# Optimization experiments

Hardware: AMD Instinct MI355X
Metric: run time of the kernel (lower is better)

## Reference

```python
import jax, jax.numpy as jnp
import numpy as np

N_NODES = 50000
N_EDGES = 800000
D_IN = 512
D_OUT = 256


def setup_inputs() -> dict:
    key = jax.random.key(0)
    k1, k2, k3 = jax.random.split(key, 3)
    x = jax.random.normal(k1, (N_NODES, D_IN), dtype=jnp.float32)
    edge_index = jax.random.randint(k2, (2, N_EDGES), 0, N_NODES, dtype=jnp.int64)
    # Glorot-style init for the GCN weight, zero bias (PyG defaults)
    W = jax.random.normal(k3, (D_IN, D_OUT), dtype=jnp.float32) * (1.0 / np.sqrt(D_IN))
    b = jnp.zeros((D_OUT,), dtype=jnp.float32)
    return {"x": x, "edge_index": edge_index, "W": W, "b": b}


def reference(x, edge_index, W, b):
    N = x.shape[0]
    # 1) dense linear transform (the compute-heavy GEMM)
    xw = x @ W  # [N, d_out]

    # 2) add self-loops (PyG GCNConv default)
    loop = jnp.arange(N, dtype=edge_index.dtype)
    row = jnp.concatenate([edge_index[0], loop])  # sources
    col = jnp.concatenate([edge_index[1], loop])  # targets

    # 3) symmetric normalization deg^{-1/2} on targets (in-degree incl. self-loops)
    deg = jax.ops.segment_sum(jnp.ones_like(col, dtype=xw.dtype), col, num_segments=N)
    dinv = jnp.where(deg > 0, jax.lax.rsqrt(deg), 0.0)
    norm = dinv[row] * dinv[col]  # [E+N]

    # 4) gather source features, scale, scatter-add to targets
    msgs = xw[row] * norm[:, None]  # [E+N, d_out]
    agg = jax.ops.segment_sum(msgs, col, num_segments=N)  # [N, d_out]

    # 5) bias + ReLU (dropout is identity in eval mode)
    return jax.nn.relu(agg + b)
```

## Files before the change

### kernel.cpp

```cpp
#include <hip/hip_runtime.h>
#include <hip/hip_bf16.h>

#define N_NODES 50000
#define N_EDGES 800000
#define D_IN    512
#define D_OUT   256
#define NBLK_SCAN ((N_NODES + 1023) / 1024)

typedef short s8v  __attribute__((ext_vector_type(8)));
typedef float f32x4 __attribute__((ext_vector_type(4)));

__device__ __forceinline__ unsigned short bf16b(float f) {
    __hip_bfloat16 h = __float2bfloat16(f);
    return *reinterpret_cast<unsigned short*>(&h);
}

__device__ __forceinline__ int wave_incl_scan(int v, int lane) {
    #pragma unroll
    for (int d = 1; d < 64; d <<= 1) {
        int u = __shfl_up(v, d, 64);
        if (lane >= d) v += u;
    }
    return v;
}


__global__ void k_count(const int* __restrict__ col, int* __restrict__ cnt) {
    int i = blockIdx.x * 256 + threadIdx.x;
    if (i < N_EDGES) atomicAdd(&cnt[col[i]], 1);
}

__launch_bounds__(256)
__global__ void k_scan1(const int* __restrict__ cnt, int* __restrict__ bsum) {
    const int t = threadIdx.x, b = blockIdx.x;
    const int idx = b * 1024 + t * 4;
    int4 v = make_int4(0, 0, 0, 0);
    if (idx < N_NODES) v = *(const int4*)&cnt[idx];
    int s = v.x + v.y + v.z + v.w;
    #pragma unroll
    for (int d = 1; d < 64; d <<= 1) s += __shfl_xor(s, d, 64);
    __shared__ int ws[4];
    if ((t & 63) == 0) ws[t >> 6] = s;
    __syncthreads();
    if (t == 0) bsum[b] = ws[0] + ws[1] + ws[2] + ws[3];
}

__global__ void k_scan2(const int* __restrict__ bsum, int* __restrict__ boff) {
    const int t = threadIdx.x;
    int v = (t < NBLK_SCAN) ? bsum[t] : 0;
    int inc = wave_incl_scan(v, t);
    if (t < NBLK_SCAN) boff[t] = inc - v;
}

__launch_bounds__(256)
__global__ void k_scan3(const int* __restrict__ cnt, const int* __restrict__ boff,
                        int* __restrict__ row_ptr, float* __restrict__ dinv,
                        int* __restrict__ cursor) {
    const int t = threadIdx.x, b = blockIdx.x;
    const int lane = t & 63, wv = t >> 6;
    const int idx = b * 1024 + t * 4;
    int4 v = make_int4(0, 0, 0, 0);
    if (idx < N_NODES) v = *(const int4*)&cnt[idx];
    int s = v.x + v.y + v.z + v.w;
    int isc = wave_incl_scan(s, lane);
    __shared__ int wsum[4];
    if (lane == 63) wsum[wv] = isc;
    __syncthreads();
    int off = boff[b];
    #pragma unroll
    for (int i = 0; i < 4; ++i)
        if (i < wv) off += wsum[i];
    int p0 = off + isc - s;
    int p1 = p0 + v.x;
    int p2 = p1 + v.y;
    int p3 = p2 + v.z;
    if (idx < N_NODES) {
        row_ptr[idx + 0] = p0; cursor[idx + 0] = p0; dinv[idx + 0] = rsqrtf(1.f + (float)v.x);
        row_ptr[idx + 1] = p1; cursor[idx + 1] = p1; dinv[idx + 1] = rsqrtf(1.f + (float)v.y);
        row_ptr[idx + 2] = p2; cursor[idx + 2] = p2; dinv[idx + 2] = rsqrtf(1.f + (float)v.z);
        row_ptr[idx + 3] = p3; cursor[idx + 3] = p3; dinv[idx + 3] = rsqrtf(1.f + (float)v.w);
    }
    if (b == 0 && t == 0) row_ptr[N_NODES] = N_EDGES;
}

__global__ void k_fill(const int* __restrict__ row, const int* __restrict__ col,
                       int* __restrict__ cursor, int* __restrict__ csr_src) {
    int i = blockIdx.x * 256 + threadIdx.x;
    if (i < N_EDGES) {
        int pos = atomicAdd(&cursor[col[i]], 1);
        csr_src[pos] = row[i];
    }
}

__global__ void k_wt(const float* __restrict__ W, unsigned short* __restrict__ Wt) {
    int k = blockIdx.x;
    int n = threadIdx.x;
    Wt[(size_t)n * D_IN + k] = bf16b(W[(size_t)k * D_OUT + n]);
}

__launch_bounds__(256)
__global__ void k_gemm(const float* __restrict__ A,
                       const unsigned short* __restrict__ Wt,
                       const float* __restrict__ dinv,
                       unsigned short* __restrict__ yb)
{
    __shared__ __align__(16) unsigned short As[128 * 64];
    __shared__ __align__(16) unsigned short Bs[128 * 64];

    const int t  = threadIdx.x;
    const int nt = blockIdx.x & 1;
    const int mt = blockIdx.x >> 1;
    const int m0 = mt * 128;
    const int n0 = nt * 128;

    const int w  = t >> 6;
    const int l  = t & 63;
    const int wm = (w >> 1) * 64;
    const int wn = (w & 1) * 64;
    const int lr = l & 15;
    const int lk = l >> 4;

    const int sr   = t >> 3;
    const int skg  = t & 7;
    const int swz  = (sr & 7) << 4;
    const int aswz = (lr & 7) << 4;

    f32x4 acc[4][4] = {};

    for (int kk = 0; kk < D_IN; kk += 64) {
        #pragma unroll
        for (int i = 0; i < 4; ++i) {
            int m   = i * 32 + sr;
            int row = m0 + m;
            float4 v0 = make_float4(0.f,0.f,0.f,0.f), v1 = v0;
            if (row < N_NODES) {
                const float* src = &A[(size_t)row * D_IN + kk + skg * 8];
                v0 = *(const float4*)src;
                v1 = *(const float4*)(src + 4);
            }
            union { uint4 q; unsigned short h[8]; } pk;
            pk.h[0] = bf16b(v0.x); pk.h[1] = bf16b(v0.y);
            pk.h[2] = bf16b(v0.z); pk.h[3] = bf16b(v0.w);
            pk.h[4] = bf16b(v1.x); pk.h[5] = bf16b(v1.y);
            pk.h[6] = bf16b(v1.z); pk.h[7] = bf16b(v1.w);
            *(uint4*)((char*)As + ((m * 128 + skg * 16) ^ swz)) = pk.q;
        }
        #pragma unroll
        for (int i = 0; i < 4; ++i) {
            int n = i * 32 + sr;
            uint4 q = *(const uint4*)&Wt[(size_t)(n0 + n) * D_IN + kk + skg * 8];
            *(uint4*)((char*)Bs + ((n * 128 + skg * 16) ^ swz)) = q;
        }
        __syncthreads();

        #pragma unroll
        for (int ks = 0; ks < 2; ++ks) {
            const int kb = (ks * 64 + lk * 16) ^ aswz;
            s8v af[4], bfr[4];
            #pragma unroll
            for (int f = 0; f < 4; ++f)
                af[f]  = *(const s8v*)((const char*)As + ((wm + f * 16 + lr) * 128 + kb));
            #pragma unroll
            for (int f = 0; f < 4; ++f)
                bfr[f] = *(const s8v*)((const char*)Bs + ((wn + f * 16 + lr) * 128 + kb));
            #pragma unroll
            for (int fm = 0; fm < 4; ++fm)
                #pragma unroll
                for (int fn = 0; fn < 4; ++fn)
                    acc[fm][fn] = __builtin_amdgcn_mfma_f32_16x16x32_bf16(
                        af[fm], bfr[fn], acc[fm][fn], 0, 0, 0);
        }
        __syncthreads();
    }

    #pragma unroll
    for (int fm = 0; fm < 4; ++fm) {
        #pragma unroll
        for (int j = 0; j < 4; ++j) {
            int row = m0 + wm + fm * 16 + lk * 4 + j;
            if (row < N_NODES) {
                float s = dinv[row];
                #pragma unroll
                for (int fn = 0; fn < 4; ++fn) {
                    int col = n0 + wn + fn * 16 + lr;
                    yb[(size_t)row * D_OUT + col] = bf16b(acc[fm][fn][j] * s);
                }
            }
        }
    }
}

__device__ __forceinline__ void add8(float* acc, uint4 q) {
    unsigned x;
    x = q.x; acc[0] += __uint_as_float(x << 16); acc[1] += __uint_as_float(x & 0xffff0000u);
    x = q.y; acc[2] += __uint_as_float(x << 16); acc[3] += __uint_as_float(x & 0xffff0000u);
    x = q.z; acc[4] += __uint_as_float(x << 16); acc[5] += __uint_as_float(x & 0xffff0000u);
    x = q.w; acc[6] += __uint_as_float(x << 16); acc[7] += __uint_as_float(x & 0xffff0000u);
}

__launch_bounds__(256)
__global__ void k_gather(const int* __restrict__ row_ptr, const int* __restrict__ csr_src,
                         const unsigned short* __restrict__ yb, const float* __restrict__ dinv,
                         const float* __restrict__ bias, float* __restrict__ out)
{
    const int c  = blockIdx.x * 4 + (threadIdx.x >> 6);
    const int l  = threadIdx.x & 63;
    const int eg = l >> 5;
    const int cs = l & 31;
    const size_t colb = (size_t)cs * 8;

    float acc[8] = {0.f,0.f,0.f,0.f,0.f,0.f,0.f,0.f};

    const int s = row_ptr[c];
    const int e = row_ptr[c + 1];

    int i = s + eg;
    while (i + 14 < e) {
        int r[8];
        #pragma unroll
        for (int u = 0; u < 8; ++u) r[u] = csr_src[i + 2 * u];
        uint4 v[8];
        #pragma unroll
        for (int u = 0; u < 8; ++u) v[u] = *(const uint4*)&yb[(size_t)r[u] * D_OUT + colb];
        #pragma unroll
        for (int u = 0; u < 8; ++u) add8(acc, v[u]);
        i += 16;
    }
    if (i + 6 < e) {
        int r[4];
        #pragma unroll
        for (int u = 0; u < 4; ++u) r[u] = csr_src[i + 2 * u];
        uint4 v[4];
        #pragma unroll
        for (int u = 0; u < 4; ++u) v[u] = *(const uint4*)&yb[(size_t)r[u] * D_OUT + colb];
        #pragma unroll
        for (int u = 0; u < 4; ++u) add8(acc, v[u]);
        i += 8;
    }
    while (i < e) {
        int r = csr_src[i];
        uint4 v = *(const uint4*)&yb[(size_t)r * D_OUT + colb];
        add8(acc, v);
        i += 2;
    }

    #pragma unroll
    for (int u = 0; u < 8; ++u) acc[u] += __shfl_xor(acc[u], 32, 64);

    uint4 sv = *(const uint4*)&yb[(size_t)c * D_OUT + colb];
    add8(acc, sv);

    if (eg == 0) {
        const float sc = dinv[c];
        float4 b0 = *(const float4*)&bias[colb];
        float4 b1 = *(const float4*)&bias[colb + 4];
        float4 o0, o1;
        o0.x = fmaxf(fmaf(acc[0], sc, b0.x), 0.f);
        o0.y = fmaxf(fmaf(acc[1], sc, b0.y), 0.f);
        o0.z = fmaxf(fmaf(acc[2], sc, b0.z), 0.f);
        o0.w = fmaxf(fmaf(acc[3], sc, b0.w), 0.f);
        o1.x = fmaxf(fmaf(acc[4], sc, b1.x), 0.f);
        o1.y = fmaxf(fmaf(acc[5], sc, b1.y), 0.f);
        o1.z = fmaxf(fmaf(acc[6], sc, b1.z), 0.f);
        o1.w = fmaxf(fmaf(acc[7], sc, b1.w), 0.f);
        float* dst = &out[(size_t)c * D_OUT + colb];
        *(float4*)dst       = o0;
        *(float4*)(dst + 4) = o1;
    }
}

extern "C" void kernel_launch(void* const* d_in, const int* in_sizes, int n_in,
                              void* d_out, int out_size, void* d_ws, size_t ws_size,
                              hipStream_t stream) {
    const float* x   = (const float*)d_in[0];
    const int*   ei  = (const int*)d_in[1];
    const float* W   = (const float*)d_in[2];
    const float* b   = (const float*)d_in[3];
    float*       out = (float*)d_out;

    const int* row = ei;
    const int* col = ei + N_EDGES;

    char* p = (char*)d_ws;
    unsigned short* yb = (unsigned short*)p;  p += (size_t)N_NODES * D_OUT * 2;
    unsigned short* Wt = (unsigned short*)p;  p += (size_t)D_OUT * D_IN * 2;
    int*   csr_src = (int*)p;                 p += (size_t)N_EDGES * 4;
    int*   cnt     = (int*)p;                 p += (size_t)N_NODES * 4;
    int*   row_ptr = (int*)p;                 p += (size_t)(N_NODES + 4) * 4;
    int*   cursor  = (int*)p;                 p += (size_t)N_NODES * 4;
    float* dinv    = (float*)p;               p += (size_t)N_NODES * 4;
    int*   bsum    = (int*)p;                 p += (size_t)NBLK_SCAN * 4;
    int*   boff    = (int*)p;                 p += (size_t)NBLK_SCAN * 4;

    hipMemsetAsync(cnt, 0, (size_t)N_NODES * sizeof(int), stream);
    k_count<<<(N_EDGES + 255) / 256, 256, 0, stream>>>(col, cnt);
    k_scan1<<<NBLK_SCAN, 256, 0, stream>>>(cnt, bsum);
    k_scan2<<<1, 64, 0, stream>>>(bsum, boff);
    k_scan3<<<NBLK_SCAN, 256, 0, stream>>>(cnt, boff, row_ptr, dinv, cursor);
    k_fill <<<(N_EDGES + 255) / 256, 256, 0, stream>>>(row, col, cursor, csr_src);
    k_wt   <<<D_IN, D_OUT, 0, stream>>>(W, Wt);

    k_gemm<<<((N_NODES + 127) / 128) * 2, 256, 0, stream>>>(x, Wt, dinv, yb);

    k_gather<<<N_NODES / 4, 256, 0, stream>>>(row_ptr, csr_src, yb, dinv, b, out);
}
```

Baseline: 228.2 us.

## Pre-convert x to scaled bf16 and load GEMM tiles via global_load_lds

Adds a separate pass that scales x by dinv and converts it to bf16, so the GEMM reads half-width data and no longer converts in its inner loop. The GEMM tile loads now go straight from global memory to LDS through global_load_lds with XOR-swizzled source columns. Workgroup IDs are also remapped so that neighbouring tiles land on the same XCD. The cost is an extra full read of x plus a write and re-read of a 51 MB bf16 copy. Rows past the end are clamped to row 0 rather than zero-filled, which is safe only because those output rows are never stored.

```diff
diff --git a/kernel.cpp b/kernel.cpp
--- a/kernel.cpp
+++ b/kernel.cpp
@@ -6,6 +6,9 @@
 #define D_IN    512
 #define D_OUT   256
 #define NBLK_SCAN ((N_NODES + 1023) / 1024)
+#define GEMM_NWG (((N_NODES + 127) / 128) * 2)
+#define GEMM_Q   (GEMM_NWG / 8)
+#define GEMM_R   (GEMM_NWG % 8)
 
 typedef short s8v  __attribute__((ext_vector_type(8)));
 typedef float f32x4 __attribute__((ext_vector_type(4)));
@@ -14,6 +17,11 @@
     __hip_bfloat16 h = __float2bfloat16(f);
     return *reinterpret_cast<unsigned short*>(&h);
 }
+
+#define GLD16(gp, lp)                                                           \
+    __builtin_amdgcn_global_load_lds(                                           \
+        (const __attribute__((address_space(1))) unsigned int*)(const void*)(gp),\
+        (__attribute__((address_space(3))) unsigned int*)(void*)(lp), 16, 0, 0)
 
 __device__ __forceinline__ int wave_incl_scan(int v, int lane) {
     #pragma unroll
@@ -99,57 +107,72 @@
 }
 
 __launch_bounds__(256)
-__global__ void k_gemm(const float* __restrict__ A,
+__global__ void k_xb(const float* __restrict__ x, const float* __restrict__ dinv,
+                     unsigned short* __restrict__ xb) {
+    int idx = blockIdx.x * 256 + threadIdx.x;
+    const int tot = N_NODES * D_IN / 8;
+    if (idx >= tot) return;
+    int node = idx >> 6;
+    float s = dinv[node];
+    const float4* src = (const float4*)x + (size_t)idx * 2;
+    float4 v0 = src[0], v1 = src[1];
+    union { uint4 q; unsigned short h[8]; } pk;
+    pk.h[0] = bf16b(v0.x * s); pk.h[1] = bf16b(v0.y * s);
+    pk.h[2] = bf16b(v0.z * s); pk.h[3] = bf16b(v0.w * s);
+    pk.h[4] = bf16b(v1.x * s); pk.h[5] = bf16b(v1.y * s);
+    pk.h[6] = bf16b(v1.z * s); pk.h[7] = bf16b(v1.w * s);
+    ((uint4*)xb)[idx] = pk.q;
+}
+
+__launch_bounds__(256)
+__global__ void k_gemm(const unsigned short* __restrict__ xb,
                        const unsigned short* __restrict__ Wt,
-                       const float* __restrict__ dinv,
                        unsigned short* __restrict__ yb)
 {
     __shared__ __align__(16) unsigned short As[128 * 64];
     __shared__ __align__(16) unsigned short Bs[128 * 64];
 
-    const int t  = threadIdx.x;
-    const int nt = blockIdx.x & 1;
-    const int mt = blockIdx.x >> 1;
+    int orig = blockIdx.x;
+    int xcd = orig % 8, pos = orig / 8;
+    int wg = (xcd < GEMM_R) ? xcd * (GEMM_Q + 1) + pos
+                            : GEMM_R * (GEMM_Q + 1) + (xcd - GEMM_R) * GEMM_Q + pos;
+    const int nt = wg & 1;
+    const int mt = wg >> 1;
     const int m0 = mt * 128;
     const int n0 = nt * 128;
 
+    const int t  = threadIdx.x;
     const int w  = t >> 6;
     const int l  = t & 63;
     const int wm = (w >> 1) * 64;
     const int wn = (w & 1) * 64;
     const int lr = l & 15;
     const int lk = l >> 4;
-
-    const int sr   = t >> 3;
-    const int skg  = t & 7;
-    const int swz  = (sr & 7) << 4;
     const int aswz = (lr & 7) << 4;
 
+    const int srow = l >> 3;
+    const int srcj = (l & 7) ^ srow;
+
+    size_t aoff[4];
+    size_t boff[4];
+    #pragma unroll
+    for (int i = 0; i < 4; ++i) {
+        int g = w * 4 + i;
+        int am = m0 + g * 8 + srow;
+        if (am >= N_NODES) am = 0;
+        aoff[i] = (size_t)am * D_IN + srcj * 8;
+        int bn = n0 + g * 8 + srow;
+        boff[i] = (size_t)bn * D_IN + srcj * 8;
+    }
+
     f32x4 acc[4][4] = {};
 
     for (int kk = 0; kk < D_IN; kk += 64) {
         #pragma unroll
         for (int i = 0; i < 4; ++i) {
-            int m   = i * 32 + sr;
-            int row = m0 + m;
-            float4 v0 = make_float4(0.f,0.f,0.f,0.f), v1 = v0;
-            if (row < N_NODES) {
-                const float* src = &A[(size_t)row * D_IN + kk + skg * 8];
-                v0 = *(const float4*)src;
-                v1 = *(const float4*)(src + 4);
-            }
-            union { uint4 q; unsigned short h[8]; } pk;
-            pk.h[0] = bf16b(v0.x); pk.h[1] = bf16b(v0.y);
-            pk.h[2] = bf16b(v0.z); pk.h[3] = bf16b(v0.w);
-            pk.h[4] = bf16b(v1.x); pk.h[5] = bf16b(v1.y);
-            pk.h[6] = bf16b(v1.z); pk.h[7] = bf16b(v1.w);
-            *(uint4*)((char*)As + ((m * 128 + skg * 16) ^ swz)) = pk.q;
-        }
-        #pragma unroll
-        for (int i = 0; i < 4; ++i) {
-            int n = i * 32 + sr;
-            uint4 q = *(const uint4*)&Wt[(size_t)(n0 + n) * D_IN + kk + skg * 8];
-            *(uint4*)((char*)Bs + ((n * 128 + skg * 16) ^ swz)) = q;
+            int g = w * 4 + i;
+            GLD16(&xb[aoff[i] + kk], (char*)As + g * 1024);
+            GLD16(&Wt[boff[i] + kk], (char*)Bs + g * 1024);
         }
         __syncthreads();
 
@@ -179,11 +202,10 @@
         for (int j = 0; j < 4; ++j) {
             int row = m0 + wm + fm * 16 + lk * 4 + j;
             if (row < N_NODES) {
-                float s = dinv[row];
                 #pragma unroll
                 for (int fn = 0; fn < 4; ++fn) {
                     int col = n0 + wn + fn * 16 + lr;
-                    yb[(size_t)row * D_OUT + col] = bf16b(acc[fm][fn][j] * s);
+                    yb[(size_t)row * D_OUT + col] = bf16b(acc[fm][fn][j]);
                 }
             }
         }
@@ -283,6 +305,7 @@
 
     char* p = (char*)d_ws;
     unsigned short* yb = (unsigned short*)p;  p += (size_t)N_NODES * D_OUT * 2;
+    unsigned short* xb = (unsigned short*)p;  p += (size_t)N_NODES * D_IN * 2;
     unsigned short* Wt = (unsigned short*)p;  p += (size_t)D_OUT * D_IN * 2;
     int*   csr_src = (int*)p;                 p += (size_t)N_EDGES * 4;
     int*   cnt     = (int*)p;                 p += (size_t)N_NODES * 4;
@@ -299,8 +322,9 @@
     k_scan3<<<NBLK_SCAN, 256, 0, stream>>>(cnt, boff, row_ptr, dinv, cursor);
     k_fill <<<(N_EDGES + 255) / 256, 256, 0, stream>>>(row, col, cursor, csr_src);
     k_wt   <<<D_IN, D_OUT, 0, stream>>>(W, Wt);
-
-    k_gemm<<<((N_NODES + 127) / 128) * 2, 256, 0, stream>>>(x, Wt, dinv, yb);
+    k_xb   <<<(N_NODES * D_IN / 8 + 255) / 256, 256, 0, stream>>>(x, dinv, xb);
+
+    k_gemm<<<GEMM_NWG, 256, 0, stream>>>(xb, Wt, yb);
 
     k_gather<<<N_NODES / 4, 256, 0, stream>>>(row_ptr, csr_src, yb, dinv, b, out);
 }
```

Measured after the change: 213.6 us. 6.4% less time.

## Double-buffer GEMM with direct global-to-LDS loads, XCD remap, and batched gather tail

Applied to the files above, without the earlier changes.

The GEMM now stages fp32 A and bf16 W tiles straight into LDS with global_load_lds, double-buffered over k-steps of 32, so the next tile's loads overlap the current MFMA work. The bf16 conversion of A moves to the LDS-read side. Workgroup IDs are remapped so neighbouring tiles land on the same XCD, which should improve L2 reuse. The gather tail is replaced by a predicated 4-wide loop to cut serial single-edge iterations. In exchange, LDS use doubles and the conversion work is repeated per wave.

```diff
diff --git a/kernel.cpp b/kernel.cpp
--- a/kernel.cpp
+++ b/kernel.cpp
@@ -6,6 +6,9 @@
 #define D_IN    512
 #define D_OUT   256
 #define NBLK_SCAN ((N_NODES + 1023) / 1024)
+#define GEMM_NWG (((N_NODES + 127) / 128) * 2)
+#define GEMM_Q   (GEMM_NWG / 8)
+#define GEMM_R   (GEMM_NWG % 8)
 
 typedef short s8v  __attribute__((ext_vector_type(8)));
 typedef float f32x4 __attribute__((ext_vector_type(4)));
@@ -14,6 +17,13 @@
     __hip_bfloat16 h = __float2bfloat16(f);
     return *reinterpret_cast<unsigned short*>(&h);
 }
+__device__ __forceinline__ float bflo(unsigned u) { return __uint_as_float(u << 16); }
+__device__ __forceinline__ float bfhi(unsigned u) { return __uint_as_float(u & 0xffff0000u); }
+
+#define GLD16(gp, lp)                                                           \
+    __builtin_amdgcn_global_load_lds(                                           \
+        (const __attribute__((address_space(1))) unsigned int*)(const void*)(gp),\
+        (__attribute__((address_space(3))) unsigned int*)(void*)(lp), 16, 0, 0)
 
 __device__ __forceinline__ int wave_incl_scan(int v, int lane) {
     #pragma unroll
@@ -104,15 +114,19 @@
                        const float* __restrict__ dinv,
                        unsigned short* __restrict__ yb)
 {
-    __shared__ __align__(16) unsigned short As[128 * 64];
-    __shared__ __align__(16) unsigned short Bs[128 * 64];
-
-    const int t  = threadIdx.x;
-    const int nt = blockIdx.x & 1;
-    const int mt = blockIdx.x >> 1;
+    __shared__ __align__(16) float          As[2 * 128 * 32];
+    __shared__ __align__(16) unsigned short Bs[2 * 128 * 32];
+
+    int orig = blockIdx.x;
+    int xcd = orig % 8, pos = orig / 8;
+    int wg = (xcd < GEMM_R) ? xcd * (GEMM_Q + 1) + pos
+                            : GEMM_R * (GEMM_Q + 1) + (xcd - GEMM_R) * GEMM_Q + pos;
+    const int nt = wg & 1;
+    const int mt = wg >> 1;
     const int m0 = mt * 128;
     const int n0 = nt * 128;
 
+    const int t  = threadIdx.x;
     const int w  = t >> 6;
     const int l  = t & 63;
     const int wm = (w >> 1) * 64;
@@ -120,58 +134,78 @@
     const int lr = l & 15;
     const int lk = l >> 4;
 
-    const int sr   = t >> 3;
-    const int skg  = t & 7;
-    const int swz  = (sr & 7) << 4;
-    const int aswz = (lr & 7) << 4;
+    size_t aoff[4];
+    #pragma unroll
+    for (int i = 0; i < 4; ++i) {
+        int r = m0 + w * 32 + i * 8 + (l >> 3);
+        if (r >= N_NODES) r = 0;
+        aoff[i] = (size_t)r * D_IN + ((l & 7) ^ (l >> 3)) * 4;
+    }
+    size_t boff[2];
+    #pragma unroll
+    for (int i = 0; i < 2; ++i) {
+        int r = n0 + w * 32 + i * 16 + (l >> 2);
+        boff[i] = (size_t)r * D_IN + ((l & 3) ^ ((l >> 3) & 3)) * 8;
+    }
 
     f32x4 acc[4][4] = {};
 
-    for (int kk = 0; kk < D_IN; kk += 64) {
-        #pragma unroll
-        for (int i = 0; i < 4; ++i) {
-            int m   = i * 32 + sr;
-            int row = m0 + m;
-            float4 v0 = make_float4(0.f,0.f,0.f,0.f), v1 = v0;
-            if (row < N_NODES) {
-                const float* src = &A[(size_t)row * D_IN + kk + skg * 8];
-                v0 = *(const float4*)src;
-                v1 = *(const float4*)(src + 4);
-            }
-            union { uint4 q; unsigned short h[8]; } pk;
-            pk.h[0] = bf16b(v0.x); pk.h[1] = bf16b(v0.y);
-            pk.h[2] = bf16b(v0.z); pk.h[3] = bf16b(v0.w);
-            pk.h[4] = bf16b(v1.x); pk.h[5] = bf16b(v1.y);
-            pk.h[6] = bf16b(v1.z); pk.h[7] = bf16b(v1.w);
-            *(uint4*)((char*)As + ((m * 128 + skg * 16) ^ swz)) = pk.q;
-        }
-        #pragma unroll
-        for (int i = 0; i < 4; ++i) {
-            int n = i * 32 + sr;
-            uint4 q = *(const uint4*)&Wt[(size_t)(n0 + n) * D_IN + kk + skg * 8];
-            *(uint4*)((char*)Bs + ((n * 128 + skg * 16) ^ swz)) = q;
-        }
+    #define STAGE(buf, kk)                                                       \
+        do {                                                                     \
+            char* ab = (char*)As + (buf) * 16384 + w * 4096;                     \
+            char* bb = (char*)Bs + (buf) * 8192  + w * 2048;                     \
+            _Pragma("unroll")                                                    \
+            for (int i = 0; i < 4; ++i) GLD16(&A[aoff[i] + (kk)], ab + i * 1024);\
+            _Pragma("unroll")                                                    \
+            for (int i = 0; i < 2; ++i) GLD16(&Wt[boff[i] + (kk)], bb + i * 1024);\
+        } while (0)
+
+    #define COMPUTE(buf)                                                         \
+        do {                                                                     \
+            const char* abase = (const char*)As + (buf) * 16384;                 \
+            const char* bbase = (const char*)Bs + (buf) * 8192;                  \
+            s8v af[4], bfr[4];                                                   \
+            _Pragma("unroll")                                                    \
+            for (int f = 0; f < 4; ++f) {                                        \
+                int row = wm + f * 16 + lr;                   \
+                int s0  = (2 * lk) ^ (lr & 7);                                   \
+                const char* pr = abase + row * 128;                              \
+                float4 x0 = *(const float4*)(pr + s0 * 16);                      \
+                float4 x1 = *(const float4*)(pr + (s0 ^ 1) * 16);                \
+                union { s8v v; unsigned short h[8]; } u;                         \
+                u.h[0] = bf16b(x0.x); u.h[1] = bf16b(x0.y);                      \
+                u.h[2] = bf16b(x0.z); u.h[3] = bf16b(x0.w);                      \
+                u.h[4] = bf16b(x1.x); u.h[5] = bf16b(x1.y);                      \
+                u.h[6] = bf16b(x1.z); u.h[7] = bf16b(x1.w);                      \
+                af[f] = u.v;                                                     \
+            }                                                                    \
+            _Pragma("unroll")                                                    \
+            for (int f = 0; f < 4; ++f) {                                        \
+                int row = wn + f * 16 + lr;         \
+                int s   = lk ^ ((lr >> 1) & 3);                                  \
+                bfr[f] = *(const s8v*)(bbase + row * 64 + s * 16);               \
+            }                                                                    \
+            _Pragma("unroll")                                                    \
+            for (int fm = 0; fm < 4; ++fm)                                       \
+                _Pragma("unroll")                                                \
+                for (int fn = 0; fn < 4; ++fn)                                   \
+                    acc[fm][fn] = __builtin_amdgcn_mfma_f32_16x16x32_bf16(       \
+                        af[fm], bfr[fn], acc[fm][fn], 0, 0, 0);                  \
+        } while (0)
+
+    STAGE(0, 0);
+    __syncthreads();
+
+    #pragma unroll 1
+    for (int tk = 0; tk < 15; ++tk) {
+        STAGE((tk + 1) & 1, (tk + 1) * 32);
+        COMPUTE(tk & 1);
         __syncthreads();
-
-        #pragma unroll
-        for (int ks = 0; ks < 2; ++ks) {
-            const int kb = (ks * 64 + lk * 16) ^ aswz;
-            s8v af[4], bfr[4];
-            #pragma unroll
-            for (int f = 0; f < 4; ++f)
-                af[f]  = *(const s8v*)((const char*)As + ((wm + f * 16 + lr) * 128 + kb));
-            #pragma unroll
-            for (int f = 0; f < 4; ++f)
-                bfr[f] = *(const s8v*)((const char*)Bs + ((wn + f * 16 + lr) * 128 + kb));
-            #pragma unroll
-            for (int fm = 0; fm < 4; ++fm)
-                #pragma unroll
-                for (int fn = 0; fn < 4; ++fn)
-                    acc[fm][fn] = __builtin_amdgcn_mfma_f32_16x16x32_bf16(
-                        af[fm], bfr[fn], acc[fm][fn], 0, 0, 0);
-        }
-        __syncthreads();
-    }
+    }
+    COMPUTE(1);
+
+    #undef STAGE
+    #undef COMPUTE
 
     #pragma unroll
     for (int fm = 0; fm < 4; ++fm) {
@@ -192,10 +226,10 @@
 
 __device__ __forceinline__ void add8(float* acc, uint4 q) {
     unsigned x;
-    x = q.x; acc[0] += __uint_as_float(x << 16); acc[1] += __uint_as_float(x & 0xffff0000u);
-    x = q.y; acc[2] += __uint_as_float(x << 16); acc[3] += __uint_as_float(x & 0xffff0000u);
-    x = q.z; acc[4] += __uint_as_float(x << 16); acc[5] += __uint_as_float(x & 0xffff0000u);
-    x = q.w; acc[6] += __uint_as_float(x << 16); acc[7] += __uint_as_float(x & 0xffff0000u);
+    x = q.x; acc[0] += bflo(x); acc[1] += bfhi(x);
+    x = q.y; acc[2] += bflo(x); acc[3] += bfhi(x);
+    x = q.z; acc[4] += bflo(x); acc[5] += bfhi(x);
+    x = q.w; acc[6] += bflo(x); acc[7] += bfhi(x);
 }
 
 __launch_bounds__(256)
@@ -226,22 +260,20 @@
         for (int u = 0; u < 8; ++u) add8(acc, v[u]);
         i += 16;
     }
-    if (i + 6 < e) {
+    while (i < e) {
         int r[4];
         #pragma unroll
-        for (int u = 0; u < 4; ++u) r[u] = csr_src[i + 2 * u];
+        for (int u = 0; u < 4; ++u) {
+            int p = i + 2 * u;
+            r[u] = csr_src[p < e ? p : e - 1];
+        }
         uint4 v[4];
         #pragma unroll
         for (int u = 0; u < 4; ++u) v[u] = *(const uint4*)&yb[(size_t)r[u] * D_OUT + colb];
         #pragma unroll
-        for (int u = 0; u < 4; ++u) add8(acc, v[u]);
+        for (int u = 0; u < 4; ++u)
+            if (i + 2 * u < e) add8(acc, v[u]);
         i += 8;
-    }
-    while (i < e) {
-        int r = csr_src[i];
-        uint4 v = *(const uint4*)&yb[(size_t)r * D_OUT + colb];
-        add8(acc, v);
-        i += 2;
     }
 
     #pragma unroll
@@ -300,7 +332,7 @@
     k_fill <<<(N_EDGES + 255) / 256, 256, 0, stream>>>(row, col, cursor, csr_src);
     k_wt   <<<D_IN, D_OUT, 0, stream>>>(W, Wt);
 
-    k_gemm<<<((N_NODES + 127) / 128) * 2, 256, 0, stream>>>(x, Wt, dinv, yb);
+    k_gemm<<<GEMM_NWG, 256, 0, stream>>>(x, Wt, dinv, yb);
 
     k_gather<<<N_NODES / 4, 256, 0, stream>>>(row_ptr, csr_src, yb, dinv, b, out);
 }
```

Result: faster. 218.7 us (-4.2%).
